# Kernel tuning notes

Measured on AMD Instinct MI355X. Metric: run time of the kernel, lower is better.

## Reference

```python
import jax, jax.numpy as jnp
import numpy as np

LEAKY_SLOPE = 0.2
LN_EPS = 1e-5
SOFTMAX_EPS = 1e-16  # PyG softmax denominator eps


def setup_inputs() -> dict:
    key = jax.random.key(0)
    ks = jax.random.split(key, 8)
    N, E, F, H, C, ED = 100000, 1600000, 64, 8, 8, 16
    s = 1.0 / np.sqrt(F)
    return {
        "x": jax.random.normal(ks[0], (N, F), jnp.float32),
        "edge_index": jax.random.randint(ks[1], (2, E), 0, N, jnp.int32),
        "edge_attr": jax.random.normal(ks[2], (E, ED), jnp.float32),
        "W_l": jax.random.normal(ks[3], (H * C, F), jnp.float32) * s,
        "b_l": jnp.zeros((H * C,), jnp.float32),
        "W_r": jax.random.normal(ks[4], (H * C, F), jnp.float32) * s,
        "b_r": jnp.zeros((H * C,), jnp.float32),
        "W_e": jax.random.normal(ks[5], (H * C, ED), jnp.float32) * (1.0 / np.sqrt(ED)),
        "att": jax.random.normal(ks[6], (1, H, C), jnp.float32) * (1.0 / np.sqrt(C)),
        "bias": jnp.zeros((H * C,), jnp.float32),
        "gamma": jnp.ones((F,), jnp.float32),
        "beta": jnp.zeros((F,), jnp.float32),
    }


def reference(x, edge_index, edge_attr, W_l, b_l, W_r, b_r, W_e, att, bias, gamma, beta):
    N, F = x.shape
    H, C = att.shape[1], att.shape[2]
    src, dst = edge_index[0], edge_index[1]  # PyG: row0=source(j), row1=target(i)

    xl = (x @ W_l.T + b_l).reshape(N, H, C)   # lin_l -> x_j side
    xr = (x @ W_r.T + b_r).reshape(N, H, C)   # lin_r -> x_i side
    e = (edge_attr @ W_e.T).reshape(-1, H, C)  # lin_edge (no bias)

    m = jax.nn.leaky_relu(xl[src] + xr[dst] + e, LEAKY_SLOPE)  # [E,H,C]
    logits = jnp.einsum('ehc,hc->eh', m, att[0])               # [E,H]

    # per-destination segment softmax
    mx = jax.ops.segment_max(logits, dst, num_segments=N)      # [N,H]
    mx = jnp.where(jnp.isfinite(mx), mx, 0.0)                  # nodes w/o in-edges
    ex = jnp.exp(logits - mx[dst])
    denom = jax.ops.segment_sum(ex, dst, num_segments=N)
    alpha = ex / (denom[dst] + SOFTMAX_EPS)                    # [E,H]; dropout is identity in eval

    agg = jax.ops.segment_sum(alpha[:, :, None] * xl[src], dst, num_segments=N)  # [N,H,C]
    out = agg.reshape(N, H * C) + bias

    h = out + x  # residual
    mu = jnp.mean(h, axis=-1, keepdims=True)
    var = jnp.mean((h - mu) ** 2, axis=-1, keepdims=True)
    hn = (h - mu) * jax.lax.rsqrt(var + LN_EPS) * gamma + beta
    return jax.nn.relu(hn)
```

## Files before the change

kernel.cpp:

```cpp
#include <hip/hip_runtime.h>

#define LEAKY 0.2f
#define LN_EPS 1e-5f
#define SM_EPS 1e-16f
#define CAP 64
#define WPAD 68

__global__ __launch_bounds__(256) void k_node_linear(
    const float* __restrict__ x,
    const float* __restrict__ Wl,
    const float* __restrict__ bl,
    const float* __restrict__ Wr,
    const float* __restrict__ br,
    float* __restrict__ xl, float* __restrict__ xr,
    int* __restrict__ deg, int N)
{
    __shared__ __align__(16) float sW[64 * WPAD];

    const int tid = threadIdx.x;

    for (int i = blockIdx.x * 256 + tid; i < N; i += gridDim.x * 256) deg[i] = 0;

    const int side = blockIdx.x & 1;
    const float* __restrict__ W  = side ? Wr : Wl;
    const float* __restrict__ bv = side ? br : bl;
    float* __restrict__ dst      = side ? xr : xl;

    for (int i = tid; i < 4096; i += 256)
        sW[(i >> 6) * WPAD + (i & 63)] = W[i];
    __syncthreads();

    const int lane = tid & 63;
    float4 wq[16];
    #pragma unroll
    for (int q = 0; q < 16; ++q)
        wq[q] = *(const float4*)&sW[lane * WPAD + q * 4];
    const float bb = bv[lane];

    const int stream0 = (blockIdx.x >> 1) * 4 + (tid >> 6);
    const int nstream = (gridDim.x >> 1) * 4;
    for (int n = stream0; n < N; n += nstream) {
        const float4* xrow = (const float4*)(x + (long long)n * 64);
        float a = bb;
        #pragma unroll
        for (int q = 0; q < 16; ++q) {
            const float4 xv = xrow[q];
            const float4 w  = wq[q];
            a = fmaf(xv.x, w.x, fmaf(xv.y, w.y, fmaf(xv.z, w.z, fmaf(xv.w, w.w, a))));
        }
        dst[(long long)n * 64 + lane] = a;
    }
}

__global__ __launch_bounds__(256) void k_bucket(
    const int* __restrict__ ei,
    int* __restrict__ deg,
    int* __restrict__ slot,
    int E)
{
    const int e = blockIdx.x * 256 + threadIdx.x;
    if (e >= E) return;
    const int dst = ei[E + e];
    const int pos = atomicAdd(deg + dst, 1);
    if (pos < CAP) slot[dst * CAP + pos] = e;
}

__global__ __launch_bounds__(256) void k_gather(
    const int* __restrict__ ei,
    const float* __restrict__ ea,
    const float* __restrict__ We,
    const float* __restrict__ att,
    const float* __restrict__ xl, const float* __restrict__ xr,
    const int* __restrict__ deg, const int* __restrict__ slot,
    const float* __restrict__ x,
    const float* __restrict__ bias, const float* __restrict__ gamma,
    const float* __restrict__ beta,
    float* __restrict__ out, int N)
{
    const int lane = threadIdx.x & 63;
    const int n = blockIdx.x * 4 + (threadIdx.x >> 6);
    if (n >= N) return;

    const float4* w4 = (const float4*)(We + lane * 16);
    const float4 w0 = w4[0], w1 = w4[1], w2 = w4[2], w3 = w4[3];
    const float attv = att[lane];
    const float xrv = xr[(long long)n * 64 + lane];

    const int d = min(deg[n], CAP);

    int veid = 0, vsrc = 0;
    if (lane < d) {
        veid = slot[(long long)n * CAP + lane];
        vsrc = ei[veid];
    }

    float acc = 0.f;
    float ns  = 0.f;

    float xlA = 0.f, xlB = 0.f;
    float4 a0, a1, a2, a3, b0, b1, b2, b3;
    a0 = a1 = a2 = a3 = b0 = b1 = b2 = b3 = make_float4(0.f, 0.f, 0.f, 0.f);

#define FETCH(j, XLV, E0, E1, E2, E3) do {                       \
        const int s_ = __shfl(vsrc, (j), 64);                    \
        const int e_ = __shfl(veid, (j), 64);                    \
        XLV = xl[(long long)s_ * 64 + lane];                     \
        const float4* p_ = (const float4*)(ea + (long long)e_ * 16); \
        E0 = p_[0]; E1 = p_[1]; E2 = p_[2]; E3 = p_[3];          \
    } while (0)

    if (d > 0) FETCH(0, xlA, a0, a1, a2, a3);
    if (d > 1) FETCH(1, xlB, b0, b1, b2, b3);

    for (int i = 0; i < d; ++i) {
        const float xlc = xlA;
        const float4 c0 = a0, c1 = a1, c2 = a2, c3 = a3;
        xlA = xlB; a0 = b0; a1 = b1; a2 = b2; a3 = b3;
        if (i + 2 < d) FETCH(i + 2, xlB, b0, b1, b2, b3);

        float ep = c0.x*w0.x + c0.y*w0.y + c0.z*w0.z + c0.w*w0.w
                 + c1.x*w1.x + c1.y*w1.y + c1.z*w1.z + c1.w*w1.w
                 + c2.x*w2.x + c2.y*w2.y + c2.z*w2.z + c2.w*w2.w
                 + c3.x*w3.x + c3.y*w3.y + c3.z*w3.z + c3.w*w3.w;
        float m = xlc + xrv + ep;
        m = (m > 0.f) ? m : LEAKY * m;
        float p = m * attv;
        p += __shfl_xor(p, 1, 64);
        p += __shfl_xor(p, 2, 64);
        p += __shfl_xor(p, 4, 64);
        const float ex = __expf(p);
        ns  += ex;
        acc = fmaf(ex, xlc, acc);
    }
#undef FETCH

    const float a = acc / (ns + SM_EPS);
    const float hv = a + bias[lane] + x[(long long)n * 64 + lane];

    float s = hv;
    #pragma unroll
    for (int off = 32; off; off >>= 1) s += __shfl_xor(s, off, 64);
    const float mu = s * (1.f / 64.f);
    const float dd = hv - mu;
    float v = dd * dd;
    #pragma unroll
    for (int off = 32; off; off >>= 1) v += __shfl_xor(v, off, 64);
    const float var = v * (1.f / 64.f);

    float hn = dd * rsqrtf(var + LN_EPS) * gamma[lane] + beta[lane];
    out[(long long)n * 64 + lane] = (hn > 0.f) ? hn : 0.f;
}

extern "C" void kernel_launch(void* const* d_in, const int* in_sizes, int n_in,
                              void* d_out, int out_size, void* d_ws, size_t ws_size,
                              hipStream_t stream) {
    (void)n_in; (void)ws_size; (void)out_size;

    const float* x     = (const float*)d_in[0];
    const int*   ei    = (const int*)d_in[1];
    const float* ea    = (const float*)d_in[2];
    const float* Wl    = (const float*)d_in[3];
    const float* bl    = (const float*)d_in[4];
    const float* Wr    = (const float*)d_in[5];
    const float* br    = (const float*)d_in[6];
    const float* We    = (const float*)d_in[7];
    const float* att   = (const float*)d_in[8];
    const float* bias  = (const float*)d_in[9];
    const float* gamma = (const float*)d_in[10];
    const float* beta  = (const float*)d_in[11];

    const int N = in_sizes[0] / 64;
    const int E = in_sizes[1] / 2;

    float* w = (float*)d_ws;
    float* xl  = w;                   w += (size_t)N * 64;
    float* xr  = w;                   w += (size_t)N * 64;
    int* deg   = (int*)w;
    int* slot  = deg + N;

    float* out = (float*)d_out;

    k_node_linear<<<2048, 256, 0, stream>>>(
        x, Wl, bl, Wr, br, xl, xr, deg, N);

    k_bucket<<<(E + 255) / 256, 256, 0, stream>>>(ei, deg, slot, E);

    k_gather<<<(N + 3) / 4, 256, 0, stream>>>(
        ei, ea, We, att, xl, xr, deg, slot, x, bias, gamma, beta, out, N);
}
```

Baseline: 714.6 us.

## Persistent gather waves with next-node prefetch; bucket four edges per thread

The gather kernel becomes persistent with a fixed grid of 2048 blocks. Each wave loops over nodes in a grid stride and prefetches the next node's degree, slot entries, xr row and source indices while it computes the current node, which hides the dependent-load latency at the start of each node. The bucket kernel now processes four edges per thread with a vectorized int4 read of destinations, cutting thread count and index-load instructions. The cost is that the fixed grid may leave the GPU less able to balance uneven degrees, and the prefetched slot read for lanes beyond the degree touches unused slot memory.

Result: slower. 748.0 us (+4.7%).

```diff
diff --git a/kernel.cpp b/kernel.cpp
--- a/kernel.cpp
+++ b/kernel.cpp
@@ -58,11 +58,26 @@
     int* __restrict__ slot,
     int E)
 {
-    const int e = blockIdx.x * 256 + threadIdx.x;
-    if (e >= E) return;
-    const int dst = ei[E + e];
-    const int pos = atomicAdd(deg + dst, 1);
-    if (pos < CAP) slot[dst * CAP + pos] = e;
+    const int base = (blockIdx.x * 256 + threadIdx.x) * 4;
+    if (base >= E) return;
+    if (((E & 3) == 0) && base + 3 < E) {
+        const int4 d4 = *(const int4*)(ei + E + base);
+        const int p0 = atomicAdd(deg + d4.x, 1);
+        const int p1 = atomicAdd(deg + d4.y, 1);
+        const int p2 = atomicAdd(deg + d4.z, 1);
+        const int p3 = atomicAdd(deg + d4.w, 1);
+        if (p0 < CAP) slot[(long long)d4.x * CAP + p0] = base;
+        if (p1 < CAP) slot[(long long)d4.y * CAP + p1] = base + 1;
+        if (p2 < CAP) slot[(long long)d4.z * CAP + p2] = base + 2;
+        if (p3 < CAP) slot[(long long)d4.w * CAP + p3] = base + 3;
+    } else {
+        const int hi = (base + 4 < E) ? base + 4 : E;
+        for (int e = base; e < hi; ++e) {
+            const int dst = ei[E + e];
+            const int pos = atomicAdd(deg + dst, 1);
+            if (pos < CAP) slot[(long long)dst * CAP + pos] = e;
+        }
+    }
 }
 
 __global__ __launch_bounds__(256) void k_gather(
@@ -78,77 +93,96 @@
     float* __restrict__ out, int N)
 {
     const int lane = threadIdx.x & 63;
-    const int n = blockIdx.x * 4 + (threadIdx.x >> 6);
-    if (n >= N) return;
+    const int wid  = blockIdx.x * 4 + (threadIdx.x >> 6);
+    const int nw   = gridDim.x * 4;
+    if (wid >= N) return;
 
     const float4* w4 = (const float4*)(We + lane * 16);
     const float4 w0 = w4[0], w1 = w4[1], w2 = w4[2], w3 = w4[3];
     const float attv = att[lane];
-    const float xrv = xr[(long long)n * 64 + lane];
-
-    const int d = min(deg[n], CAP);
-
+
+    int n = wid;
+    int d = min(deg[n], CAP);
     int veid = 0, vsrc = 0;
     if (lane < d) {
         veid = slot[(long long)n * CAP + lane];
         vsrc = ei[veid];
     }
-
-    float acc = 0.f;
-    float ns  = 0.f;
-
-    float xlA = 0.f, xlB = 0.f;
-    float4 a0, a1, a2, a3, b0, b1, b2, b3;
-    a0 = a1 = a2 = a3 = b0 = b1 = b2 = b3 = make_float4(0.f, 0.f, 0.f, 0.f);
-
-#define FETCH(j, XLV, E0, E1, E2, E3) do {                       \
-        const int s_ = __shfl(vsrc, (j), 64);                    \
-        const int e_ = __shfl(veid, (j), 64);                    \
-        XLV = xl[(long long)s_ * 64 + lane];                     \
-        const float4* p_ = (const float4*)(ea + (long long)e_ * 16); \
-        E0 = p_[0]; E1 = p_[1]; E2 = p_[2]; E3 = p_[3];          \
-    } while (0)
-
-    if (d > 0) FETCH(0, xlA, a0, a1, a2, a3);
-    if (d > 1) FETCH(1, xlB, b0, b1, b2, b3);
-
-    for (int i = 0; i < d; ++i) {
-        const float xlc = xlA;
-        const float4 c0 = a0, c1 = a1, c2 = a2, c3 = a3;
-        xlA = xlB; a0 = b0; a1 = b1; a2 = b2; a3 = b3;
-        if (i + 2 < d) FETCH(i + 2, xlB, b0, b1, b2, b3);
-
-        float ep = c0.x*w0.x + c0.y*w0.y + c0.z*w0.z + c0.w*w0.w
-                 + c1.x*w1.x + c1.y*w1.y + c1.z*w1.z + c1.w*w1.w
-                 + c2.x*w2.x + c2.y*w2.y + c2.z*w2.z + c2.w*w2.w
-                 + c3.x*w3.x + c3.y*w3.y + c3.z*w3.z + c3.w*w3.w;
-        float m = xlc + xrv + ep;
-        m = (m > 0.f) ? m : LEAKY * m;
-        float p = m * attv;
-        p += __shfl_xor(p, 1, 64);
-        p += __shfl_xor(p, 2, 64);
-        p += __shfl_xor(p, 4, 64);
-        const float ex = __expf(p);
-        ns  += ex;
-        acc = fmaf(ex, xlc, acc);
-    }
+    float xrv = xr[(long long)n * 64 + lane];
+
+    for (;;) {
+        const int next = n + nw;
+        const int pn = (next < N) ? next : n;
+        const int   degN  = deg[pn];
+        const int   slotN = slot[(long long)pn * CAP + lane];
+        const float xrvN  = xr[(long long)pn * 64 + lane];
+
+        float acc = 0.f;
+        float ns  = 0.f;
+
+        float xlA = 0.f, xlB = 0.f;
+        float4 a0, a1, a2, a3, b0, b1, b2, b3;
+        a0 = a1 = a2 = a3 = b0 = b1 = b2 = b3 = make_float4(0.f, 0.f, 0.f, 0.f);
+
+#define FETCH(j, XLV, E0, E1, E2, E3) do {                           \
+            const int s_ = __shfl(vsrc, (j), 64);                    \
+            const int e_ = __shfl(veid, (j), 64);                    \
+            XLV = xl[(long long)s_ * 64 + lane];                     \
+            const float4* p_ = (const float4*)(ea + (long long)e_ * 16); \
+            E0 = p_[0]; E1 = p_[1]; E2 = p_[2]; E3 = p_[3];          \
+        } while (0)
+
+        if (d > 0) FETCH(0, xlA, a0, a1, a2, a3);
+        if (d > 1) FETCH(1, xlB, b0, b1, b2, b3);
+
+        for (int i = 0; i < d; ++i) {
+            const float xlc = xlA;
+            const float4 c0 = a0, c1 = a1, c2 = a2, c3 = a3;
+            xlA = xlB; a0 = b0; a1 = b1; a2 = b2; a3 = b3;
+            if (i + 2 < d) FETCH(i + 2, xlB, b0, b1, b2, b3);
+
+            float ep = c0.x*w0.x + c0.y*w0.y + c0.z*w0.z + c0.w*w0.w
+                     + c1.x*w1.x + c1.y*w1.y + c1.z*w1.z + c1.w*w1.w
+                     + c2.x*w2.x + c2.y*w2.y + c2.z*w2.z + c2.w*w2.w
+                     + c3.x*w3.x + c3.y*w3.y + c3.z*w3.z + c3.w*w3.w;
+            float m = xlc + xrv + ep;
+            m = (m > 0.f) ? m : LEAKY * m;
+            float p = m * attv;
+            p += __shfl_xor(p, 1, 64);
+            p += __shfl_xor(p, 2, 64);
+            p += __shfl_xor(p, 4, 64);
+            const float ex = __expf(p);
+            ns  += ex;
+            acc = fmaf(ex, xlc, acc);
+        }
 #undef FETCH
 
-    const float a = acc / (ns + SM_EPS);
-    const float hv = a + bias[lane] + x[(long long)n * 64 + lane];
-
-    float s = hv;
-    #pragma unroll
-    for (int off = 32; off; off >>= 1) s += __shfl_xor(s, off, 64);
-    const float mu = s * (1.f / 64.f);
-    const float dd = hv - mu;
-    float v = dd * dd;
-    #pragma unroll
-    for (int off = 32; off; off >>= 1) v += __shfl_xor(v, off, 64);
-    const float var = v * (1.f / 64.f);
-
-    float hn = dd * rsqrtf(var + LN_EPS) * gamma[lane] + beta[lane];
-    out[(long long)n * 64 + lane] = (hn > 0.f) ? hn : 0.f;
+        const int dN = min(degN, CAP);
+        int veidN = 0, vsrcN = 0;
+        if (next < N && lane < dN) {
+            veidN = slotN;
+            vsrcN = ei[veidN];
+        }
+
+        const float a = acc / (ns + SM_EPS);
+        const float hv = a + bias[lane] + x[(long long)n * 64 + lane];
+
+        float s = hv;
+        #pragma unroll
+        for (int off = 32; off; off >>= 1) s += __shfl_xor(s, off, 64);
+        const float mu = s * (1.f / 64.f);
+        const float dd = hv - mu;
+        float v = dd * dd;
+        #pragma unroll
+        for (int off = 32; off; off >>= 1) v += __shfl_xor(v, off, 64);
+        const float var = v * (1.f / 64.f);
+
+        float hn = dd * rsqrtf(var + LN_EPS) * gamma[lane] + beta[lane];
+        out[(long long)n * 64 + lane] = (hn > 0.f) ? hn : 0.f;
+
+        if (next >= N) break;
+        n = next; d = dN; veid = veidN; vsrc = vsrcN; xrv = xrvN;
+    }
 }
 
 extern "C" void kernel_launch(void* const* d_in, const int* in_sizes, int n_in,
@@ -183,8 +217,9 @@
     k_node_linear<<<2048, 256, 0, stream>>>(
         x, Wl, bl, Wr, br, xl, xr, deg, N);
 
-    k_bucket<<<(E + 255) / 256, 256, 0, stream>>>(ei, deg, slot, E);
-
-    k_gather<<<(N + 3) / 4, 256, 0, stream>>>(
+    const int t2 = (E + 3) / 4;
+    k_bucket<<<(t2 + 255) / 256, 256, 0, stream>>>(ei, deg, slot, E);
+
+    k_gather<<<2048, 256, 0, stream>>>(
         ei, ea, We, att, xl, xr, deg, slot, x, bias, gamma, beta, out, N);
 }
```

## Replace global atomic edge bucketing with two-pass shared-memory binned counting sort

Applied to the files above, without the earlier changes.

Replaces the per-edge global atomicAdd bucketing by destination with a two-level counting sort. First, chunks of edges are binned into coarse bins of 256 destinations using LDS histograms and a block-level scan. Second, each bin is sorted locally into per-node slot lists, so edges land in sorted order. This aims to cut global atomic contention and scattered writes, at the cost of an extra kernel, an intermediate bin array and a capacity limit (BCAP) that can silently drop edges. The deg zeroing moves from k_node_linear to a hipMemsetAsync.

After: 629.7 us. -11.9%, faster.

```diff
diff --git a/kernel.cpp b/kernel.cpp
--- a/kernel.cpp
+++ b/kernel.cpp
@@ -5,6 +5,11 @@
 #define SM_EPS 1e-16f
 #define CAP 64
 #define WPAD 68
+
+#define BIN_SHIFT 8
+#define MAXBINS   448
+#define CHUNK_A   7168
+#define BCAP      5120
 
 __global__ __launch_bounds__(256) void k_node_linear(
     const float* __restrict__ x,
@@ -12,15 +17,11 @@
     const float* __restrict__ bl,
     const float* __restrict__ Wr,
     const float* __restrict__ br,
-    float* __restrict__ xl, float* __restrict__ xr,
-    int* __restrict__ deg, int N)
+    float* __restrict__ xl, float* __restrict__ xr, int N)
 {
     __shared__ __align__(16) float sW[64 * WPAD];
 
     const int tid = threadIdx.x;
-
-    for (int i = blockIdx.x * 256 + tid; i < N; i += gridDim.x * 256) deg[i] = 0;
-
     const int side = blockIdx.x & 1;
     const float* __restrict__ W  = side ? Wr : Wl;
     const float* __restrict__ bv = side ? br : bl;
@@ -53,16 +54,136 @@
 }
 
 __global__ __launch_bounds__(256) void k_bucket(
-    const int* __restrict__ ei,
-    int* __restrict__ deg,
-    int* __restrict__ slot,
-    int E)
+    const int* __restrict__ ei, int* __restrict__ deg,
+    int* __restrict__ slot, int E)
 {
     const int e = blockIdx.x * 256 + threadIdx.x;
     if (e >= E) return;
     const int dst = ei[E + e];
     const int pos = atomicAdd(deg + dst, 1);
-    if (pos < CAP) slot[dst * CAP + pos] = e;
+    if (pos < CAP) slot[(long long)dst * CAP + pos] = e;
+}
+
+__global__ __launch_bounds__(256) void k_binA(
+    const int* __restrict__ ei,
+    int* __restrict__ binCnt,
+    int2* __restrict__ binArr,
+    int E, int nbins)
+{
+    __shared__ int2 ord[CHUNK_A];
+    __shared__ int cnt[MAXBINS], offs[MAXBINS], cur[MAXBINS], resB[MAXBINS];
+
+    const int tid  = threadIdx.x;
+    const int lane = tid & 63;
+    const int ebase = blockIdx.x * CHUNK_A;
+    const int nE = (E - ebase < CHUNK_A) ? (E - ebase) : CHUNK_A;
+    const int* __restrict__ dstp = ei + E + ebase;
+
+    for (int b = tid; b < MAXBINS; b += 256) { cnt[b] = 0; cur[b] = 0; }
+    __syncthreads();
+
+    for (int i = tid; i < nE; i += 256)
+        atomicAdd(&cnt[dstp[i] >> BIN_SHIFT], 1);
+    __syncthreads();
+
+    if (tid < 64) {
+        int carry = 0;
+        #pragma unroll
+        for (int seg = 0; seg < MAXBINS / 64; ++seg) {
+            const int v = cnt[seg * 64 + lane];
+            int s = v;
+            #pragma unroll
+            for (int off = 1; off < 64; off <<= 1) {
+                const int t = __shfl_up(s, off, 64);
+                if (lane >= off) s += t;
+            }
+            offs[seg * 64 + lane] = carry + s - v;
+            carry += __shfl(s, 63, 64);
+        }
+    }
+    __syncthreads();
+
+    for (int i = tid; i < nE; i += 256) {
+        const int d = dstp[i];
+        const int b = d >> BIN_SHIFT;
+        const int pos = atomicAdd(&cur[b], 1);
+        ord[offs[b] + pos] = make_int2(ebase + i, d);
+    }
+    __syncthreads();
+
+    for (int b = tid; b < nbins; b += 256) {
+        const int c = cnt[b];
+        resB[b] = c ? atomicAdd(&binCnt[b], c) : 0;
+    }
+    __syncthreads();
+
+    for (int i = tid; i < nE; i += 256) {
+        const int2 p = ord[i];
+        const int b = p.y >> BIN_SHIFT;
+        const int k = resB[b] + (i - offs[b]);
+        if (k < BCAP) binArr[(long long)b * BCAP + k] = p;
+    }
+}
+
+__global__ __launch_bounds__(256) void k_binB(
+    const int* __restrict__ binCnt,
+    const int2* __restrict__ binArr,
+    int* __restrict__ deg,
+    int* __restrict__ slot,
+    int N)
+{
+    __shared__ int ord2[BCAP];
+    __shared__ int cnt2[256], offs2[256], cur2[256];
+
+    const int b = blockIdx.x;
+    const int tid  = threadIdx.x;
+    const int lane = tid & 63;
+    const int dst0 = b << BIN_SHIFT;
+    int nb = binCnt[b];
+    if (nb > BCAP) nb = BCAP;
+    const int2* __restrict__ src = binArr + (long long)b * BCAP;
+
+    cnt2[tid] = 0; cur2[tid] = 0;
+    __syncthreads();
+
+    for (int i = tid; i < nb; i += 256)
+        atomicAdd(&cnt2[src[i].y - dst0], 1);
+    __syncthreads();
+
+    if (tid < 64) {
+        int carry = 0;
+        #pragma unroll
+        for (int seg = 0; seg < 4; ++seg) {
+            const int v = cnt2[seg * 64 + lane];
+            int s = v;
+            #pragma unroll
+            for (int off = 1; off < 64; off <<= 1) {
+                const int t = __shfl_up(s, off, 64);
+                if (lane >= off) s += t;
+            }
+            offs2[seg * 64 + lane] = carry + s - v;
+            carry += __shfl(s, 63, 64);
+        }
+    }
+    __syncthreads();
+
+    for (int i = tid; i < nb; i += 256) {
+        const int2 p = src[i];
+        const int d = p.y - dst0;
+        const int pos = atomicAdd(&cur2[d], 1);
+        ord2[offs2[d] + pos] = p.x;
+    }
+    __syncthreads();
+
+    const int nd = (N - dst0 < 256) ? (N - dst0) : 256;
+    if (tid < nd) deg[dst0 + tid] = cnt2[tid];
+
+    const int wv = tid >> 6;
+    for (int d = wv; d < nd; d += 4) {
+        int c = cnt2[d];
+        if (c > CAP) c = CAP;
+        if (lane < c) slot[(long long)(dst0 + d) * CAP + lane] = ord2[offs2[d] + lane];
+    }
 }
 
 __global__ __launch_bounds__(256) void k_gather(
@@ -154,7 +275,7 @@
 extern "C" void kernel_launch(void* const* d_in, const int* in_sizes, int n_in,
                               void* d_out, int out_size, void* d_ws, size_t ws_size,
                               hipStream_t stream) {
-    (void)n_in; (void)ws_size; (void)out_size;
+    (void)n_in; (void)out_size;
 
     const float* x     = (const float*)d_in[0];
     const int*   ei    = (const int*)d_in[1];
@@ -171,19 +292,32 @@
 
     const int N = in_sizes[0] / 64;
     const int E = in_sizes[1] / 2;
+    const int nbins = (N + (1 << BIN_SHIFT) - 1) >> BIN_SHIFT;
 
     float* w = (float*)d_ws;
-    float* xl  = w;                   w += (size_t)N * 64;
-    float* xr  = w;                   w += (size_t)N * 64;
-    int* deg   = (int*)w;
-    int* slot  = deg + N;
+    float* xl   = w;                      w += (size_t)N * 64;
+    float* xr   = w;                      w += (size_t)N * 64;
+    int* deg    = (int*)w;
+    int* binCnt = deg + N;
+    int* slot   = binCnt + MAXBINS;
+    int2* binArr = (int2*)(slot + (size_t)N * CAP);
+    const size_t needed = ((char*)(binArr + (size_t)nbins * BCAP)) - (char*)d_ws;
 
     float* out = (float*)d_out;
 
-    k_node_linear<<<2048, 256, 0, stream>>>(
-        x, Wl, bl, Wr, br, xl, xr, deg, N);
-
-    k_bucket<<<(E + 255) / 256, 256, 0, stream>>>(ei, deg, slot, E);
+    const bool binned = (nbins <= MAXBINS) && (ws_size >= needed);
+
+    hipMemsetAsync(deg, 0, ((size_t)N + MAXBINS) * sizeof(int), stream);
+
+    k_node_linear<<<2048, 256, 0, stream>>>(x, Wl, bl, Wr, br, xl, xr, N);
+
+    if (binned) {
+        const int nbA = (E + CHUNK_A - 1) / CHUNK_A;
+        k_binA<<<nbA, 256, 0, stream>>>(ei, binCnt, binArr, E, nbins);
+        k_binB<<<nbins, 256, 0, stream>>>(binCnt, binArr, deg, slot, N);
+    } else {
+        k_bucket<<<(E + 255) / 256, 256, 0, stream>>>(ei, deg, slot, E);
+    }
 
     k_gather<<<(N + 3) / 4, 256, 0, stream>>>(
         ei, ea, We, att, xl, xr, deg, slot, x, bias, gamma, beta, out, N);
```
